# Optimization experiments

Hardware: AMD Instinct MI355X
Metric: run time of the kernel (lower is better)

Reference implementation:

```python
import jax, jax.numpy as jnp
import numpy as np

B, T, S, L = 1, 2048, 512, 1024
C, H, Hk, D = 2048, 16, 4, 128
THETA = 10000.0


def setup_inputs() -> dict:
    key = jax.random.key(0)
    ks = jax.random.split(key, 9)
    sd = 0.02
    return {
        "x": jax.random.normal(ks[0], (B, T, C), jnp.float32),
        "stm": jax.random.normal(ks[1], (B, S, C), jnp.float32),
        "long_q": jax.random.normal(ks[2], (B, L, H, D), jnp.float32),
        "long_k": jax.random.normal(ks[3], (B, L, Hk, D), jnp.float32),
        "long_v": jax.random.normal(ks[4], (B, L, Hk, D), jnp.float32),
        "Wq": jax.random.normal(ks[5], (C, C), jnp.float32) * sd,
        "Wk": jax.random.normal(ks[6], (C, Hk * D), jnp.float32) * sd,
        "Wv": jax.random.normal(ks[7], (C, Hk * D), jnp.float32) * sd,
        "Wo": jax.random.normal(ks[8], (C, C), jnp.float32) * sd,
    }


def _rope_cos_sin(n, d, theta):
    # precompute_freqs_cis: freqs over even dims, angles t*freq
    freqs = 1.0 / (theta ** (jnp.arange(0, d, 2, dtype=jnp.float32) / d))
    ang = jnp.arange(n, dtype=jnp.float32)[:, None] * freqs[None, :]  # (n, d/2)
    return jnp.cos(ang), jnp.sin(ang)


def _apply_rope(x, cos, sin):
    # x: (B, n, h, D); complex-pair rotation over consecutive dims
    x1, x2 = x[..., 0::2], x[..., 1::2]
    c = cos[None, :, None, :]
    s = sin[None, :, None, :]
    r1 = x1 * c - x2 * s
    r2 = x1 * s + x2 * c
    return jnp.stack([r1, r2], axis=-1).reshape(x.shape)


def reference(x, stm, long_q, long_k, long_v, Wq, Wk, Wv, Wo):
    Bb, Tt, Cc = x.shape
    Ss, Ll = stm.shape[1], long_q.shape[1]
    seq = jnp.concatenate([stm, x], axis=1)  # (B, S+T, C)
    q = jnp.concatenate([long_q, (seq @ Wq).reshape(Bb, Ss + Tt, H, D)], axis=1)
    k = jnp.concatenate([long_k, (seq @ Wk).reshape(Bb, Ss + Tt, Hk, D)], axis=1)
    v = jnp.concatenate([long_v, (seq @ Wv).reshape(Bb, Ss + Tt, Hk, D)], axis=1)
    # inline RoPE on the last T+S positions only (memory bank keeps fixed encoding)
    cos, sin = _rope_cos_sin(Ss + Tt, D, THETA)
    q = q.at[:, Ll:].set(_apply_rope(q[:, Ll:], cos, sin))
    k = k.at[:, Ll:].set(_apply_rope(k[:, Ll:], cos, sin))
    tot = Ll + Ss + Tt
    # structured memory mask: causal over full stream, memory keys (< L+S) visible to all
    idx = jnp.arange(tot)
    mask = (idx[None, :] <= idx[:, None]) | (idx[None, :] < Ll + Ss)  # (tot, tot)
    # GQA: repeat_interleave kv heads
    rep = H // Hk
    kr = jnp.repeat(k, rep, axis=2)  # (B, tot, H, D)
    vr = jnp.repeat(v, rep, axis=2)
    att = jnp.einsum("bihd,bjhd->bhij", q, kr) * (1.0 / np.sqrt(D))
    att = jnp.where(mask[None, None], att, -jnp.inf)
    att = jax.nn.softmax(att, axis=-1)
    y = jnp.einsum("bhij,bjhd->bihd", att, vr).reshape(Bb, tot, Cc)
    y = y[:, -Tt:]  # keep only current-block outputs
    return y @ Wo
```

## Files before the change

### kernel.cpp

```cpp
#include <hip/hip_runtime.h>
#include <hip/hip_bf16.h>

typedef __attribute__((ext_vector_type(8))) short short8;
typedef __attribute__((ext_vector_type(4))) short short4v;
typedef __attribute__((ext_vector_type(4))) float f32x4;
typedef __attribute__((ext_vector_type(4))) float float4v;
typedef __attribute__((ext_vector_type(4))) int i32x4;

#define DEVFN static __device__ __forceinline__

#define T_N   2048
#define S_N   512
#define L_N   1024
#define C_N   2048
#define H_N   16
#define HK_N  4
#define D_N   128
#define ST_N  2560
#define TOT_N 3584
#define KV_N  512

DEVFN short f2bf(float f) {
  union { float f; unsigned u; } v; v.f = f;
  return (short)((v.u + 0x7FFFu + ((v.u >> 16) & 1u)) >> 16);
}
DEVFN float bf2f(short s) {
  union { unsigned u; float f; } v; v.u = ((unsigned)(unsigned short)s) << 16;
  return v.f;
}
DEVFN void gload16(const void* g, void* l) {
  __builtin_amdgcn_global_load_lds(
      (__attribute__((address_space(1))) void*)(g),
      (__attribute__((address_space(3))) void*)(l), 16, 0, 0);
}

#define Q_A (S_N * C_N / 4)
#define Q_B (Q_A + T_N * C_N / 4)
#define Q_C (Q_B + L_N * KV_N / 4)
#define Q_D (Q_C + L_N * KV_N / 4)
#define TAB_E (Q_D + ST_N * 64)
__global__ void k_setup(const float* __restrict__ x, const float* __restrict__ stm,
                        const float* __restrict__ lk, const float* __restrict__ lv,
                        short* __restrict__ seq, short* __restrict__ Kf,
                        short* __restrict__ Vf, float* __restrict__ ct,
                        float* __restrict__ st_) {
  int i = blockIdx.x * 256 + threadIdx.x;
  if (i < Q_D) {
    const float* src; short* dst; int off;
    if (i < Q_A)      { src = stm; dst = seq;                         off = i; }
    else if (i < Q_B) { src = x;   dst = seq + (size_t)S_N * C_N;     off = i - Q_A; }
    else if (i < Q_C) { src = lk;  dst = Kf;                          off = i - Q_B; }
    else              { src = lv;  dst = Vf;                          off = i - Q_C; }
    float4v v = reinterpret_cast<const float4v*>(src)[off];
    short4v o;
    o[0] = f2bf(v[0]); o[1] = f2bf(v[1]); o[2] = f2bf(v[2]); o[3] = f2bf(v[3]);
    reinterpret_cast<short4v*>(dst)[off] = o;
  } else {
    int j = i - Q_D;
    int p = j >> 6, fq = j & 63;
    float freq = expf(-(float)fq * (logf(10000.0f) / 64.0f));
    float ang = (float)p * freq;
    ct[j] = cosf(ang);
    st_[j] = sinf(ang);
  }
}

__global__ void k_tconv_all(const float* __restrict__ Wq, const float* __restrict__ Wk,
                            const float* __restrict__ Wv, const float* __restrict__ Wo,
                            short* __restrict__ WqT, short* __restrict__ WkT,
                            short* __restrict__ WvT, short* __restrict__ WoT) {
  __shared__ float tile[32][33];
  const int z = blockIdx.z;
  const float* in = (z == 0) ? Wq : (z == 1) ? Wk : (z == 2) ? Wv : Wo;
  short* outp     = (z == 0) ? WqT : (z == 1) ? WkT : (z == 2) ? WvT : WoT;
  const int cols = (z == 1 || z == 2) ? KV_N : C_N;
  if (blockIdx.x * 32 >= cols) return;
  int c0 = blockIdx.x * 32, r0 = blockIdx.y * 32;
  int tx = threadIdx.x, ty = threadIdx.y;
#pragma unroll
  for (int i = 0; i < 4; i++)
    tile[ty + i * 8][tx] = in[(size_t)(r0 + ty + i * 8) * cols + c0 + tx];
  __syncthreads();
#pragma unroll
  for (int i = 0; i < 4; i++)
    outp[(size_t)(c0 + ty + i * 8) * C_N + r0 + tx] = f2bf(tile[tx][ty + i * 8]);
}

__global__ void k_tv(const short* __restrict__ vf, short* __restrict__ vt) {
  __shared__ short tile[32][33];
  int hk = blockIdx.z;
  int r0 = blockIdx.x * 32;
  int d0 = blockIdx.y * 32;
  int tx = threadIdx.x, ty = threadIdx.y;
#pragma unroll
  for (int i = 0; i < 4; i++)
    tile[ty + i * 8][tx] = vf[(size_t)(r0 + ty + i * 8) * KV_N + hk * D_N + d0 + tx];
  __syncthreads();
  short* o = vt + (size_t)hk * D_N * TOT_N;
#pragma unroll
  for (int i = 0; i < 4; i++)
    o[(size_t)(d0 + ty + i * 8) * TOT_N + r0 + tx] = tile[tx][ty + i * 8];
}

__global__ __launch_bounds__(256) void k_gemm_o(
    const short* __restrict__ A, const short* __restrict__ Bt,
    float* __restrict__ C) {
  __shared__ short lbuf[2 * 6144];
  const int tid = threadIdx.x;
  const int w = tid >> 6, l = tid & 63;
  const int l15 = l & 15, lh = l >> 4;
  const int f0 = blockIdx.x;
  const int f = ((f0 & 7) << 6) + (f0 >> 3);
  const int rb = (f >> 4) << 6, cb = (f & 15) << 7;
  const int wr = (w >> 1) << 5, wc = (w & 1) << 6;
  f32x4 acc[2][4] = {};
  const int cA = tid;
  const short* pa = &A[(size_t)(rb + (cA >> 2)) * 2048 + (((cA ^ (cA >> 2)) & 3) << 3)];
  const int cB0 = tid, cB1 = 256 + tid;
  const short* pb0 = &Bt[(size_t)(cb + (cB0 >> 2)) * 2048 + (((cB0 ^ (cB0 >> 2)) & 3) << 3)];
  const short* pb1 = &Bt[(size_t)(cb + (cB1 >> 2)) * 2048 + (((cB1 ^ (cB1 >> 2)) & 3) << 3)];
  const int offA  = (w * 64) << 4;
  const int offB0 = 4096 + ((w * 64) << 4);
  const int offB1 = 4096 + ((256 + w * 64) << 4);
  char* lbase = (char*)lbuf;
  const int sw = (lh ^ (l15 & 3)) << 3;
  gload16(pa,  lbase + offA);
  gload16(pb0, lbase + offB0);
  gload16(pb1, lbase + offB1);
  int cur = 0;
  for (int kt = 0; kt < 2048; kt += 32) {
    const bool more = (kt + 32 < 2048);
    if (more) {
      char* p = lbase + (cur ^ 1) * 12288;
      gload16(pa  + kt + 32, p + offA);
      gload16(pb0 + kt + 32, p + offB0);
      gload16(pb1 + kt + 32, p + offB1);
      asm volatile("s_waitcnt vmcnt(3)" ::: "memory");
    } else {
      asm volatile("s_waitcnt vmcnt(0)" ::: "memory");
    }
    __builtin_amdgcn_s_barrier();
    __builtin_amdgcn_sched_barrier(0);
    const short* la = (const short*)(lbase + cur * 12288);
    const short* lb = (const short*)(lbase + cur * 12288 + 4096);
    short8 af[2], bg[4];
#pragma unroll
    for (int m = 0; m < 2; m++)
      af[m] = *reinterpret_cast<const short8*>(&la[(wr + m * 16 + l15) * 32 + sw]);
#pragma unroll
    for (int n = 0; n < 4; n++)
      bg[n] = *reinterpret_cast<const short8*>(&lb[(wc + n * 16 + l15) * 32 + sw]);
    __builtin_amdgcn_s_setprio(1);
#pragma unroll
    for (int m = 0; m < 2; m++)
#pragma unroll
      for (int n = 0; n < 4; n++)
        acc[m][n] = __builtin_amdgcn_mfma_f32_16x16x32_bf16(af[m], bg[n], acc[m][n], 0, 0, 0);
    __builtin_amdgcn_s_setprio(0);
    asm volatile("s_waitcnt lgkmcnt(0)" ::: "memory");
    __builtin_amdgcn_sched_barrier(0);
    __builtin_amdgcn_s_barrier();
    __builtin_amdgcn_sched_barrier(0);
    cur ^= 1;
  }
#pragma unroll
  for (int m = 0; m < 2; m++)
#pragma unroll
    for (int n = 0; n < 4; n++)
#pragma unroll
      for (int r = 0; r < 4; r++) {
        int row = rb + wr + m * 16 + lh * 4 + r;
        int col = cb + wc + n * 16 + l15;
        C[(size_t)row * 2048 + col] = acc[m][n][r];
      }
}

__global__ __launch_bounds__(256) void k_gemm_qkv(
    const short* __restrict__ A, const short* __restrict__ Bt,
    short* __restrict__ qbuf, short* __restrict__ Kf, short* __restrict__ Vf,
    const float* __restrict__ ct, const float* __restrict__ st_) {
  __shared__ short lbuf[2 * 6144];
  const int tid = threadIdx.x;
  const int w = tid >> 6, l = tid & 63;
  const int l15 = l & 15, lh = l >> 4;
  const int f0 = blockIdx.x;
  const int f = (f0 % 8) * 104 + f0 / 8;
  int rb, cb;
  if (f < 512) {
    cb = (f & 15) << 7;
    rb = 512 + ((f >> 4) << 6);
  } else {
    int g = f - 512;
    cb = (16 + (g & 7)) << 7;
    rb = (g >> 3) << 6;
  }
  const int wr = (w >> 1) << 5, wc = (w & 1) << 6;
  f32x4 acc[2][4] = {};
  const int cA = tid;
  const short* pa = &A[(size_t)(rb + (cA >> 2)) * 2048 + (((cA ^ (cA >> 2)) & 3) << 3)];
  const int cB0 = tid, cB1 = 256 + tid;
  const short* pb0 = &Bt[(size_t)(cb + (cB0 >> 2)) * 2048 + (((cB0 ^ (cB0 >> 2)) & 3) << 3)];
  const short* pb1 = &Bt[(size_t)(cb + (cB1 >> 2)) * 2048 + (((cB1 ^ (cB1 >> 2)) & 3) << 3)];
  const int offA  = (w * 64) << 4;
  const int offB0 = 4096 + ((w * 64) << 4);
  const int offB1 = 4096 + ((256 + w * 64) << 4);
  char* lbase = (char*)lbuf;
  const int sw = (lh ^ (l15 & 3)) << 3;
  gload16(pa,  lbase + offA);
  gload16(pb0, lbase + offB0);
  gload16(pb1, lbase + offB1);
  int cur = 0;
  for (int kt = 0; kt < 2048; kt += 32) {
    const bool more = (kt + 32 < 2048);
    if (more) {
      char* p = lbase + (cur ^ 1) * 12288;
      gload16(pa  + kt + 32, p + offA);
      gload16(pb0 + kt + 32, p + offB0);
      gload16(pb1 + kt + 32, p + offB1);
      asm volatile("s_waitcnt vmcnt(3)" ::: "memory");
    } else {
      asm volatile("s_waitcnt vmcnt(0)" ::: "memory");
    }
    __builtin_amdgcn_s_barrier();
    __builtin_amdgcn_sched_barrier(0);
    const short* la = (const short*)(lbase + cur * 12288);
    const short* lb = (const short*)(lbase + cur * 12288 + 4096);
    short8 af[2], bg[4];
#pragma unroll
    for (int m = 0; m < 2; m++)
      af[m] = *reinterpret_cast<const short8*>(&la[(wr + m * 16 + l15) * 32 + sw]);
#pragma unroll
    for (int n = 0; n < 4; n++)
      bg[n] = *reinterpret_cast<const short8*>(&lb[(wc + n * 16 + l15) * 32 + sw]);
    __builtin_amdgcn_s_setprio(1);
#pragma unroll
    for (int m = 0; m < 2; m++)
#pragma unroll
      for (int n = 0; n < 4; n++)
        acc[m][n] = __builtin_amdgcn_mfma_f32_16x16x32_bf16(af[m], bg[n], acc[m][n], 0, 0, 0);
    __builtin_amdgcn_s_setprio(0);
    asm volatile("s_waitcnt lgkmcnt(0)" ::: "memory");
    __builtin_amdgcn_sched_barrier(0);
    __builtin_amdgcn_s_barrier();
    __builtin_amdgcn_sched_barrier(0);
    cur ^= 1;
  }
#pragma unroll
  for (int m = 0; m < 2; m++)
#pragma unroll
    for (int n = 0; n < 4; n++) {
      int coln = cb + wc + n * 16 + l15;
      const bool do_rope = coln < 2560;
      const int fidx = (coln & 127) >> 1;
#pragma unroll
      for (int r = 0; r < 4; r++) {
        int row = rb + wr + m * 16 + lh * 4 + r;
        float v = acc[m][n][r];
        float other = __shfl_xor(v, 1, 64);
        if (do_rope) {
          float co = ct[row * 64 + fidx];
          float si = st_[row * 64 + fidx];
          v = (l15 & 1) ? (other * si + v * co) : (v * co - other * si);
        }
        short bv = f2bf(v);
        if (coln < 2048) {
          if (row >= 512) qbuf[(size_t)(row - 512) * C_N + coln] = bv;
        } else if (coln < 2560) {
          Kf[(size_t)(L_N + row) * KV_N + (coln - 2048)] = bv;
        } else {
          Vf[(size_t)(L_N + row) * KV_N + (coln - 2560)] = bv;
        }
      }
    }
}

__global__ __launch_bounds__(256, 2) void k_attn(
    const short* __restrict__ Q,
    const short* __restrict__ Kf,
    const short* __restrict__ Vt,
    short* __restrict__ pY,
    float* __restrict__ pM,
    float* __restrict__ pL) {
  __shared__ short kl[64 * 128];
  __shared__ short vl[128 * 64];
  const int f = blockIdx.x;
  const int p = f >> 8;
  const int f8 = f & 255;
  const int hk = f8 & 3;
  const int qraw = (f8 >> 2) & 15;
  const int hh = (f8 >> 6) & 3;
  const int qb = p ? (15 - qraw) : qraw;
  const int h = hk * 4 + hh;
  const int tid = threadIdx.x, w = tid >> 6, l = tid & 63;
  const int l15 = l & 15, lh = l >> 4;
  const int qbase = qb << 7;
  const int qrow0 = qbase + (w << 5);
  short8 aqA[4], aqB[4];
#pragma unroll
  for (int kb = 0; kb < 4; kb++) {
    aqA[kb] = *reinterpret_cast<const short8*>(
        &Q[(size_t)(qrow0 + l15) * C_N + h * D_N + kb * 32 + lh * 8]);
    aqB[kb] = *reinterpret_cast<const short8*>(
        &Q[(size_t)(qrow0 + 16 + l15) * C_N + h * D_N + kb * 32 + lh * 8]);
  }
  short8 ones;
#pragma unroll
  for (int j = 0; j < 8; j++) ones[j] = (short)0x3F80;
  f32x4 yA[8] = {}, yB[8] = {};
  f32x4 lA_ = {}, lB_ = {};
  float mA = -3.0e38f, mB = -3.0e38f;
  const float K2 = 0.12751744f;
  const float THR = 90.0f;
  const int nkt = ((qbase + 1663) >> 6) + 1;
  const int th = nkt >> 1;
  const int t0 = p ? th : 0;
  const int t1 = p ? nkt : th;
  const short* psk[4];
  const short* psv[4];
  int ldsoff[4];
#pragma unroll
  for (int it = 0; it < 4; it++) {
    int c = it * 256 + tid;
    int kr = c >> 4, kkc = c & 15;
    int pkr = (kr & 0x23) | ((kr & 0x0C) << 1) | ((kr >> 2) & 4);
    psk[it] = &Kf[(size_t)pkr * KV_N + hk * D_N + ((kkc ^ (kr & 7)) << 3)];
    int vrow = c >> 3, vkc = c & 7;
    psv[it] = &Vt[(size_t)hk * D_N * TOT_N + (size_t)vrow * TOT_N + ((vkc ^ (vrow & 7)) << 3)];
    ldsoff[it] = (it * 256 + w * 64) << 4;
  }
#pragma unroll
  for (int it = 0; it < 4; it++)
    gload16(psk[it] + (size_t)t0 * 64 * KV_N, (char*)kl + ldsoff[it]);
#pragma unroll
  for (int it = 0; it < 4; it++)
    gload16(psv[it] + (size_t)t0 * 64, (char*)vl + ldsoff[it]);
  __syncthreads();
  for (int t = t0; t < t1; t++) {
    const bool more = (t + 1 < t1);
    short8 kreg[4], vreg[4];
    if (more) {
#pragma unroll
      for (int it = 0; it < 4; it++)
        kreg[it] = *reinterpret_cast<const short8*>(psk[it] + (size_t)(t + 1) * 64 * KV_N);
#pragma unroll
      for (int it = 0; it < 4; it++)
        vreg[it] = *reinterpret_cast<const short8*>(psv[it] + (size_t)(t + 1) * 64);
    }
    f32x4 sA[4] = {}, sB[4] = {};
    __builtin_amdgcn_s_setprio(1);
#pragma unroll
    for (int g = 0; g < 4; g++) {
      int row = g * 16 + l15;
#pragma unroll
      for (int kb = 0; kb < 4; kb++) {
        short8 bk = *reinterpret_cast<const short8*>(
            (const char*)kl + row * 256 + ((((kb << 2) + lh) ^ (row & 7)) << 4));
        sA[g] = __builtin_amdgcn_mfma_f32_16x16x32_bf16(bk, aqA[kb], sA[g], 0, 0, 0);
        sB[g] = __builtin_amdgcn_mfma_f32_16x16x32_bf16(bk, aqB[kb], sB[g], 0, 0, 0);
      }
    }
    __builtin_amdgcn_s_setprio(0);
    if ((t * 64 + 63) > (1536 + qrow0)) {
      int qi = qrow0 + l15;
#pragma unroll
      for (int g = 0; g < 4; g++)
#pragma unroll
        for (int r = 0; r < 4; r++) {
          int key = t * 64 + ((g >> 1) << 5) + (lh << 3) + ((g & 1) << 2) + r;
          if (key > 1536 + qi) sA[g][r] = -3.0e38f;
        }
    }
    if ((t * 64 + 63) > (1536 + qrow0 + 16)) {
      int qi = qrow0 + 16 + l15;
#pragma unroll
      for (int g = 0; g < 4; g++)
#pragma unroll
        for (int r = 0; r < 4; r++) {
          int key = t * 64 + ((g >> 1) << 5) + (lh << 3) + ((g & 1) << 2) + r;
          if (key > 1536 + qi) sB[g][r] = -3.0e38f;
        }
    }
    {
      float lm = sA[0][0];
#pragma unroll
      for (int g = 0; g < 4; g++)
#pragma unroll
        for (int r = 0; r < 4; r++) lm = fmaxf(lm, sA[g][r]);
      if (!__all(lm <= mA + THR)) {
        float rm = fmaxf(lm, __shfl_xor(lm, 16, 64));
        rm = fmaxf(rm, __shfl_xor(rm, 32, 64));
        float mn = fmaxf(mA, rm);
        float scf = __builtin_amdgcn_exp2f((mA - mn) * K2);
        mA = mn;
#pragma unroll
        for (int r = 0; r < 4; r++) {
          float sc_c = __shfl(scf, lh * 4 + r, 64);
          lA_[r] *= sc_c;
#pragma unroll
          for (int dg = 0; dg < 8; dg++) yA[dg][r] *= sc_c;
        }
      }
    }
    {
      float lm = sB[0][0];
#pragma unroll
      for (int g = 0; g < 4; g++)
#pragma unroll
        for (int r = 0; r < 4; r++) lm = fmaxf(lm, sB[g][r]);
      if (!__all(lm <= mB + THR)) {
        float rm = fmaxf(lm, __shfl_xor(lm, 16, 64));
        rm = fmaxf(rm, __shfl_xor(rm, 32, 64));
        float mn = fmaxf(mB, rm);
        float scf = __builtin_amdgcn_exp2f((mB - mn) * K2);
        mB = mn;
#pragma unroll
        for (int r = 0; r < 4; r++) {
          float sc_c = __shfl(scf, lh * 4 + r, 64);
          lB_[r] *= sc_c;
#pragma unroll
          for (int dg = 0; dg < 8; dg++) yB[dg][r] *= sc_c;
        }
      }
    }
    union { i32x4 wv; short8 sv; } uA0, uA1, uB0, uB1;
    {
      const float mk = mA * K2;
      float pvv[16];
#pragma unroll
      for (int g = 0; g < 4; g++)
#pragma unroll
        for (int r = 0; r < 4; r++)
          pvv[g * 4 + r] = __builtin_amdgcn_exp2f(sA[g][r] * K2 - mk);
#pragma unroll
      for (int j = 0; j < 4; j++) {
        unsigned w0, w1;
        int b0 = (j >> 1) * 4 + 2 * (j & 1);
        int b1 = (2 + (j >> 1)) * 4 + 2 * (j & 1);
        asm("v_cvt_pk_bf16_f32 %0, %1, %2" : "=v"(w0) : "v"(pvv[b0]), "v"(pvv[b0 + 1]));
        asm("v_cvt_pk_bf16_f32 %0, %1, %2" : "=v"(w1) : "v"(pvv[b1]), "v"(pvv[b1 + 1]));
        uA0.wv[j] = (int)w0;
        uA1.wv[j] = (int)w1;
      }
    }
    {
      const float mk = mB * K2;
      float pvv[16];
#pragma unroll
      for (int g = 0; g < 4; g++)
#pragma unroll
        for (int r = 0; r < 4; r++)
          pvv[g * 4 + r] = __builtin_amdgcn_exp2f(sB[g][r] * K2 - mk);
#pragma unroll
      for (int j = 0; j < 4; j++) {
        unsigned w0, w1;
        int b0 = (j >> 1) * 4 + 2 * (j & 1);
        int b1 = (2 + (j >> 1)) * 4 + 2 * (j & 1);
        asm("v_cvt_pk_bf16_f32 %0, %1, %2" : "=v"(w0) : "v"(pvv[b0]), "v"(pvv[b0 + 1]));
        asm("v_cvt_pk_bf16_f32 %0, %1, %2" : "=v"(w1) : "v"(pvv[b1]), "v"(pvv[b1 + 1]));
        uB0.wv[j] = (int)w0;
        uB1.wv[j] = (int)w1;
      }
    }
    lA_ = __builtin_amdgcn_mfma_f32_16x16x32_bf16(uA0.sv, ones, lA_, 0, 0, 0);
    lA_ = __builtin_amdgcn_mfma_f32_16x16x32_bf16(uA1.sv, ones, lA_, 0, 0, 0);
    lB_ = __builtin_amdgcn_mfma_f32_16x16x32_bf16(uB0.sv, ones, lB_, 0, 0, 0);
    lB_ = __builtin_amdgcn_mfma_f32_16x16x32_bf16(uB1.sv, ones, lB_, 0, 0, 0);
    __builtin_amdgcn_s_setprio(1);
#pragma unroll
    for (int dg = 0; dg < 8; dg++) {
      int vrow = dg * 16 + l15;
      short8 bv0 = *reinterpret_cast<const short8*>(
          (const char*)vl + (vrow << 7) + ((lh ^ (vrow & 7)) << 4));
      short8 bv1 = *reinterpret_cast<const short8*>(
          (const char*)vl + (vrow << 7) + (((4 + lh) ^ (vrow & 7)) << 4));
      yA[dg] = __builtin_amdgcn_mfma_f32_16x16x32_bf16(uA0.sv, bv0, yA[dg], 0, 0, 0);
      yA[dg] = __builtin_amdgcn_mfma_f32_16x16x32_bf16(uA1.sv, bv1, yA[dg], 0, 0, 0);
      yB[dg] = __builtin_amdgcn_mfma_f32_16x16x32_bf16(uB0.sv, bv0, yB[dg], 0, 0, 0);
      yB[dg] = __builtin_amdgcn_mfma_f32_16x16x32_bf16(uB1.sv, bv1, yB[dg], 0, 0, 0);
    }
    __builtin_amdgcn_s_setprio(0);
    asm volatile("s_waitcnt lgkmcnt(0)" ::: "memory");
    __builtin_amdgcn_sched_barrier(0);
    __builtin_amdgcn_s_barrier();
    __builtin_amdgcn_sched_barrier(0);
    if (more) {
#pragma unroll
      for (int it = 0; it < 4; it++)
        *reinterpret_cast<short8*>((char*)kl + ldsoff[it] + (l << 4)) = kreg[it];
#pragma unroll
      for (int it = 0; it < 4; it++)
        *reinterpret_cast<short8*>((char*)vl + ldsoff[it] + (l << 4)) = vreg[it];
    }
    __syncthreads();
  }
  const size_t base = (size_t)(p * 16 + h) * 2048;
#pragma unroll
  for (int dg = 0; dg < 8; dg++)
#pragma unroll
    for (int r = 0; r < 4; r++) {
      int rowA = qrow0 + lh * 4 + r;
      pY[(base + rowA) * 128 + dg * 16 + l15] = f2bf(yA[dg][r]);
      pY[(base + rowA + 16) * 128 + dg * 16 + l15] = f2bf(yB[dg][r]);
    }
  if (l15 == 0) {
#pragma unroll
    for (int r = 0; r < 4; r++) {
      pL[base + qrow0 + lh * 4 + r] = lA_[r];
      pL[base + qrow0 + 16 + lh * 4 + r] = lB_[r];
    }
  }
  if (lh == 0) {
    pM[base + qrow0 + l15] = mA;
    pM[base + qrow0 + 16 + l15] = mB;
  }
}

__global__ void k_merge(const short* __restrict__ pY, const float* __restrict__ pM,
                        const float* __restrict__ pL, short* __restrict__ Y) {
  const int h = blockIdx.y;
  const int row = blockIdx.x * 16 + (threadIdx.x >> 4);
  const int d0 = (threadIdx.x & 15) * 8;
  const size_t b0 = (size_t)h * 2048 + row;
  const size_t b1 = (size_t)(16 + h) * 2048 + row;
  const float K2 = 0.12751744f;
  float m0 = pM[b0], m1 = pM[b1];
  float l0 = pL[b0], l1 = pL[b1];
  float M = fmaxf(m0, m1);
  float a0 = __builtin_amdgcn_exp2f((m0 - M) * K2);
  float a1 = __builtin_amdgcn_exp2f((m1 - M) * K2);
  float inv = 1.0f / (l0 * a0 + l1 * a1);
  short8 y0 = *reinterpret_cast<const short8*>(&pY[b0 * 128 + d0]);
  short8 y1 = *reinterpret_cast<const short8*>(&pY[b1 * 128 + d0]);
  short8 o;
#pragma unroll
  for (int j = 0; j < 8; j++)
    o[j] = f2bf((bf2f(y0[j]) * a0 + bf2f(y1[j]) * a1) * inv);
  *reinterpret_cast<short8*>(&Y[(size_t)row * C_N + h * D_N + d0]) = o;
}

extern "C" void kernel_launch(void* const* d_in, const int* in_sizes, int n_in,
                              void* d_out, int out_size, void* d_ws, size_t ws_size,
                              hipStream_t stream) {
  const float* x      = (const float*)d_in[0];
  const float* stm    = (const float*)d_in[1];
  const float* long_k = (const float*)d_in[3];
  const float* long_v = (const float*)d_in[4];
  const float* Wq     = (const float*)d_in[5];
  const float* Wk     = (const float*)d_in[6];
  const float* Wv     = (const float*)d_in[7];
  const float* Wo     = (const float*)d_in[8];
  float* out = (float*)d_out;

  short* seq  = (short*)d_ws;
  short* WqT  = seq  + (size_t)ST_N * C_N;
  short* WkT  = WqT  + (size_t)C_N * C_N;
  short* WvT  = WkT  + (size_t)KV_N * C_N;
  short* WoT  = WvT  + (size_t)KV_N * C_N;
  short* qbuf = WoT  + (size_t)C_N * C_N;
  short* Kf   = qbuf + (size_t)T_N * C_N;
  short* Vf   = Kf   + (size_t)TOT_N * KV_N;
  short* Vt   = Vf   + (size_t)TOT_N * KV_N;
  short* ybuf = Vt   + (size_t)TOT_N * KV_N;
  float* ctab = (float*)(ybuf + (size_t)T_N * C_N);
  float* stab = ctab + (size_t)ST_N * 64;

  short* pY = (short*)d_ws;
  float* pM = (float*)(pY + (size_t)2 * 16 * 2048 * 128);
  float* pL = pM + (size_t)2 * 16 * 2048;

  k_setup<<<TAB_E / 256, 256, 0, stream>>>(x, stm, long_k, long_v, seq, Kf, Vf, ctab, stab);

  k_tconv_all<<<dim3(64, 64, 4), dim3(32, 8), 0, stream>>>(
      Wq, Wk, Wv, Wo, WqT, WkT, WvT, WoT);

  k_gemm_qkv<<<832, 256, 0, stream>>>(seq, WqT, qbuf, Kf, Vf, ctab, stab);

  k_tv<<<dim3(TOT_N / 32, D_N / 32, HK_N), dim3(32, 8), 0, stream>>>(Vf, Vt);

  k_attn<<<512, 256, 0, stream>>>(qbuf, Kf, Vt, pY, pM, pL);

  k_merge<<<dim3(128, 16), 256, 0, stream>>>(pY, pM, pL, ybuf);

  k_gemm_o<<<512, 256, 0, stream>>>(ybuf, WoT, out);
}
```

Before: 176.9 us.

## Enlarge QKV GEMM tiles to 256x128 with 512-thread blocks

The QKV projection GEMM switches from 64x128 tiles with 256 threads to 256x128 tiles with 512 threads (8 waves, each computing a 64x64 sub-tile), cutting the grid from 832 to 208 blocks. Each block now loads two A chunks and one B chunk per k-step, raising arithmetic intensity and reducing B-tile reloads across row blocks. Q tiles now start at row 512, so the per-element row guard is dropped. The cost is fewer blocks than a 256-CU device can fill, doubled LDS per block and higher accumulator register pressure.

```diff
diff --git a/kernel.cpp b/kernel.cpp
--- a/kernel.cpp
+++ b/kernel.cpp
@@ -175,66 +175,65 @@
       }
 }
 
-__global__ __launch_bounds__(256) void k_gemm_qkv(
+__global__ __launch_bounds__(512, 2) void k_gemm_qkv(
     const short* __restrict__ A, const short* __restrict__ Bt,
     short* __restrict__ qbuf, short* __restrict__ Kf, short* __restrict__ Vf,
     const float* __restrict__ ct, const float* __restrict__ st_) {
-  __shared__ short lbuf[2 * 6144];
+  __shared__ short lbuf[2 * 12288];
   const int tid = threadIdx.x;
   const int w = tid >> 6, l = tid & 63;
   const int l15 = l & 15, lh = l >> 4;
   const int f0 = blockIdx.x;
-  const int f = (f0 % 8) * 104 + f0 / 8;
+  const int f = (f0 % 8) * 26 + f0 / 8;
   int rb, cb;
-  if (f < 512) {
+  if (f < 128) {
+    rb = 512 + ((f >> 4) << 8);
     cb = (f & 15) << 7;
-    rb = 512 + ((f >> 4) << 6);
   } else {
-    int g = f - 512;
-    cb = (16 + (g & 7)) << 7;
-    rb = (g >> 3) << 6;
-  }
-  const int wr = (w >> 1) << 5, wc = (w & 1) << 6;
-  f32x4 acc[2][4] = {};
-  const int cA = tid;
-  const short* pa = &A[(size_t)(rb + (cA >> 2)) * 2048 + (((cA ^ (cA >> 2)) & 3) << 3)];
-  const int cB0 = tid, cB1 = 256 + tid;
-  const short* pb0 = &Bt[(size_t)(cb + (cB0 >> 2)) * 2048 + (((cB0 ^ (cB0 >> 2)) & 3) << 3)];
-  const short* pb1 = &Bt[(size_t)(cb + (cB1 >> 2)) * 2048 + (((cB1 ^ (cB1 >> 2)) & 3) << 3)];
-  const int offA  = (w * 64) << 4;
-  const int offB0 = 4096 + ((w * 64) << 4);
-  const int offB1 = 4096 + ((256 + w * 64) << 4);
+    int g = f - 128;
+    rb = (g >> 3) << 8;
+    cb = 2048 + ((g & 7) << 7);
+  }
+  const int wr = (w >> 1) << 6, wc = (w & 1) << 6;
+  f32x4 acc[4][4] = {};
+  const int cA0 = tid, cA1 = 512 + tid;
+  const short* pa0 = &A[(size_t)(rb + (cA0 >> 2)) * 2048 + (((cA0 ^ (cA0 >> 2)) & 3) << 3)];
+  const short* pa1 = &A[(size_t)(rb + (cA1 >> 2)) * 2048 + (((cA1 ^ (cA1 >> 2)) & 3) << 3)];
+  const short* pb = &Bt[(size_t)(cb + (tid >> 2)) * 2048 + (((tid ^ (tid >> 2)) & 3) << 3)];
+  const int offA0 = (w * 64) << 4;
+  const int offA1 = (512 + w * 64) << 4;
+  const int offB  = 16384 + ((w * 64) << 4);
   char* lbase = (char*)lbuf;
   const int sw = (lh ^ (l15 & 3)) << 3;
-  gload16(pa,  lbase + offA);
-  gload16(pb0, lbase + offB0);
-  gload16(pb1, lbase + offB1);
+  gload16(pa0, lbase + offA0);
+  gload16(pa1, lbase + offA1);
+  gload16(pb,  lbase + offB);
   int cur = 0;
   for (int kt = 0; kt < 2048; kt += 32) {
     const bool more = (kt + 32 < 2048);
     if (more) {
-      char* p = lbase + (cur ^ 1) * 12288;
-      gload16(pa  + kt + 32, p + offA);
-      gload16(pb0 + kt + 32, p + offB0);
-      gload16(pb1 + kt + 32, p + offB1);
+      char* p = lbase + (cur ^ 1) * 24576;
+      gload16(pa0 + kt + 32, p + offA0);
+      gload16(pa1 + kt + 32, p + offA1);
+      gload16(pb  + kt + 32, p + offB);
       asm volatile("s_waitcnt vmcnt(3)" ::: "memory");
     } else {
       asm volatile("s_waitcnt vmcnt(0)" ::: "memory");
     }
     __builtin_amdgcn_s_barrier();
     __builtin_amdgcn_sched_barrier(0);
-    const short* la = (const short*)(lbase + cur * 12288);
-    const short* lb = (const short*)(lbase + cur * 12288 + 4096);
-    short8 af[2], bg[4];
-#pragma unroll
-    for (int m = 0; m < 2; m++)
+    const short* la = (const short*)(lbase + cur * 24576);
+    const short* lb = (const short*)(lbase + cur * 24576 + 16384);
+    short8 af[4], bg[4];
+#pragma unroll
+    for (int m = 0; m < 4; m++)
       af[m] = *reinterpret_cast<const short8*>(&la[(wr + m * 16 + l15) * 32 + sw]);
 #pragma unroll
     for (int n = 0; n < 4; n++)
       bg[n] = *reinterpret_cast<const short8*>(&lb[(wc + n * 16 + l15) * 32 + sw]);
     __builtin_amdgcn_s_setprio(1);
 #pragma unroll
-    for (int m = 0; m < 2; m++)
+    for (int m = 0; m < 4; m++)
 #pragma unroll
       for (int n = 0; n < 4; n++)
         acc[m][n] = __builtin_amdgcn_mfma_f32_16x16x32_bf16(af[m], bg[n], acc[m][n], 0, 0, 0);
@@ -246,7 +245,7 @@
     cur ^= 1;
   }
 #pragma unroll
-  for (int m = 0; m < 2; m++)
+  for (int m = 0; m < 4; m++)
 #pragma unroll
     for (int n = 0; n < 4; n++) {
       int coln = cb + wc + n * 16 + l15;
@@ -264,7 +263,7 @@
         }
         short bv = f2bf(v);
         if (coln < 2048) {
-          if (row >= 512) qbuf[(size_t)(row - 512) * C_N + coln] = bv;
+          qbuf[(size_t)(row - 512) * C_N + coln] = bv;
         } else if (coln < 2560) {
           Kf[(size_t)(L_N + row) * KV_N + (coln - 2048)] = bv;
         } else {
@@ -573,7 +572,7 @@
   k_tconv_all<<<dim3(64, 64, 4), dim3(32, 8), 0, stream>>>(
       Wq, Wk, Wv, Wo, WqT, WkT, WvT, WoT);
 
-  k_gemm_qkv<<<832, 256, 0, stream>>>(seq, WqT, qbuf, Kf, Vf, ctab, stab);
+  k_gemm_qkv<<<208, 512, 0, stream>>>(seq, WqT, qbuf, Kf, Vf, ctab, stab);
 
   k_tv<<<dim3(TOT_N / 32, D_N / 32, HK_N), dim3(32, 8), 0, stream>>>(Vf, Vt);
 
```

After: 169.7 us (median of 2 runs). 1.04x faster.
